# Optimization experiments

Hardware: AMD Instinct MI355X
Metric: run time of the kernel (lower is better)

## Reference

```python
import jax, jax.numpy as jnp
import numpy as np

RADIUS = 0.5
K = 32  # num_neighbor


def ball_query(distances, radius, k):
    # distances: (B, M, N) squared distances; mark points outside radius with N,
    # then sort indices so in-range points (in original order) come first.
    B, M, N = distances.shape
    idx = jnp.where(distances >= radius ** 2, N,
                    jnp.arange(N, dtype=jnp.int32)[None, None, :])
    return jnp.sort(idx, axis=-1)[:, :, :k]  # (B, M, k), padded with N


def setup_inputs() -> dict:
    key = jax.random.key(0)
    ks = jax.random.split(key, 6)
    B, N, M, D, C = 4, 16384, 1024, 3, 64
    C_op, C_out = 64, 128
    positions = jax.random.normal(ks[0], (B, N, D), jnp.float32)
    features = jax.random.normal(ks[1], (B, N, C), jnp.float32)
    centers = jax.random.normal(ks[2], (B, M, D), jnp.float32)
    distances = jax.random.uniform(ks[3], (B, M, N), dtype=jnp.float32)
    W_op = jax.random.normal(ks[4], (D + C, C_op), jnp.float32) * 0.05
    b_op = jnp.zeros((C_op,), jnp.float32)
    W_agg = jax.random.normal(ks[5], (C_op, C_out), jnp.float32) * 0.05
    b_agg = jnp.zeros((C_out,), jnp.float32)
    return {"positions": positions, "features": features, "centers": centers,
            "distances": distances, "W_op": W_op, "b_op": b_op,
            "W_agg": W_agg, "b_agg": b_agg}


def reference(positions, features, centers, distances, W_op, b_op, W_agg, b_agg):
    B, N, D = positions.shape
    ids = ball_query(distances, RADIUS, K)      # (B, M, K); N marks invalid slot
    mask = ids != N                             # valid neighbor mask
    safe = jnp.where(mask, ids, 0)
    bidx = jnp.arange(B)[:, None, None]
    pos_n = positions[bidx, safe]               # (B, M, K, D) neighbor gather
    feat_n = features[bidx, safe]               # (B, M, K, C)
    rel = pos_n - centers[:, :, None, :]        # relative coordinates
    # NeighborOperator: pointwise linear on [rel_pos, features]
    f = jnp.concatenate([rel, feat_n], axis=-1) @ W_op + b_op  # (B, M, K, C_op)
    # invalid slots map to the zeros row in the torch index_put trick
    f = jnp.where(mask[..., None], f, 0.0)
    pooled = jnp.max(f, axis=2)                 # neighbor max-pool (B, M, C_op)
    # Conv1dBlock with kernel 1 == per-center linear + relu
    return jax.nn.relu(pooled @ W_agg + b_agg)  # (B, M, out_channels)
```

## Files before the change

kernel.cpp:

```cpp
#include <hip/hip_runtime.h>

constexpr int B_   = 4;
constexpr int N_   = 16384;
constexpr int M_   = 1024;
constexpr int C_   = 64;
constexpr int CIN_ = 3 + C_;
constexpr int COP_ = 64;
constexpr int COUT_ = 128;
constexpr int K_   = 32;
constexpr float R2_ = 0.25f;

__global__ __launch_bounds__(64) void pointnet_fused(
    const float* __restrict__ positions,
    const float* __restrict__ features,
    const float* __restrict__ centers,
    const float* __restrict__ distances,
    const float* __restrict__ W_op,
    const float* __restrict__ b_op,
    const float* __restrict__ W_agg,
    const float* __restrict__ b_agg,
    float* __restrict__ out)
{
    const int j  = threadIdx.x;
    const int bm = blockIdx.x;
    const int b  = bm >> 10;

    __shared__ int   s_ids[K_];
    __shared__ float s_pooled[COP_];

    float w[CIN_];
    #pragma unroll
    for (int c = 0; c < CIN_; ++c) w[c] = W_op[c * COP_ + j];
    const float bop_j = b_op[j];

    const float ctr0 = centers[bm * 3 + 0];
    const float ctr1 = centers[bm * 3 + 1];
    const float ctr2 = centers[bm * 3 + 2];

    const float* drow = distances + (size_t)bm * N_;
    int found = 0;
    for (int n0 = 0; n0 < N_ && found < K_; n0 += 64) {
        const float d = drow[n0 + j];
        const bool pred = d < R2_;
        const unsigned long long mask = __ballot(pred);
        const int rank = found + __popcll(mask & ((1ull << j) - 1ull));
        if (pred && rank < K_) s_ids[rank] = n0 + j;
        found += (int)__popcll(mask);
    }
    const int valid = found < K_ ? found : K_;
    __syncthreads();

    float pooled = -INFINITY;
    for (int k = 0; k < valid; ++k) {
        const int id = __builtin_amdgcn_readfirstlane(s_ids[k]);
        const float* pp = positions + ((size_t)b * N_ + id) * 3;
        const float* fp = features  + ((size_t)b * N_ + id) * C_;
        float acc = bop_j;
        acc = fmaf(pp[0] - ctr0, w[0], acc);
        acc = fmaf(pp[1] - ctr1, w[1], acc);
        acc = fmaf(pp[2] - ctr2, w[2], acc);
        #pragma unroll
        for (int c = 0; c < C_; ++c) acc = fmaf(fp[c], w[3 + c], acc);
        pooled = fmaxf(pooled, acc);
    }
    if (valid < K_) pooled = fmaxf(pooled, 0.0f);

    s_pooled[j] = pooled;
    __syncthreads();

    float acc0 = b_agg[j];
    float acc1 = b_agg[j + 64];
    #pragma unroll
    for (int jj = 0; jj < COP_; ++jj) {
        const float p = s_pooled[jj];
        acc0 = fmaf(p, W_agg[jj * COUT_ + j],      acc0);
        acc1 = fmaf(p, W_agg[jj * COUT_ + j + 64], acc1);
    }
    float* orow = out + (size_t)bm * COUT_;
    orow[j]      = fmaxf(acc0, 0.0f);
    orow[j + 64] = fmaxf(acc1, 0.0f);
}

extern "C" void kernel_launch(void* const* d_in, const int* in_sizes, int n_in,
                              void* d_out, int out_size, void* d_ws, size_t ws_size,
                              hipStream_t stream) {
    const float* positions = (const float*)d_in[0];
    const float* features  = (const float*)d_in[1];
    const float* centers   = (const float*)d_in[2];
    const float* distances = (const float*)d_in[3];
    const float* W_op      = (const float*)d_in[4];
    const float* b_op      = (const float*)d_in[5];
    const float* W_agg     = (const float*)d_in[6];
    const float* b_agg     = (const float*)d_in[7];
    float* out = (float*)d_out;

    dim3 grid(B_ * M_);
    dim3 block(64);
    pointnet_fused<<<grid, block, 0, stream>>>(
        positions, features, centers, distances,
        W_op, b_op, W_agg, b_agg, out);
}
```

Before: 341.0 us.

## Stage neighbor features in LDS via coalesced gather and pack four centers per block

Gathers the 32 neighbor feature rows with coalesced per-lane loads into shared memory, plus relative positions, instead of serial scalar loads per channel. The neighbor MLP then reads float4 rows from LDS, and every slot is computed and masked to zero when invalid. Four centers share a 256-thread block, which cuts block count and amortises the weight loads. In exchange it uses more LDS and registers and always computes all 32 slots.

```diff
diff --git a/kernel.cpp b/kernel.cpp
--- a/kernel.cpp
+++ b/kernel.cpp
@@ -1,16 +1,17 @@
 #include <hip/hip_runtime.h>
 
-constexpr int B_   = 4;
-constexpr int N_   = 16384;
-constexpr int M_   = 1024;
-constexpr int C_   = 64;
-constexpr int CIN_ = 3 + C_;
-constexpr int COP_ = 64;
+constexpr int B_    = 4;
+constexpr int N_    = 16384;
+constexpr int M_    = 1024;
+constexpr int C_    = 64;
+constexpr int CIN_  = 68;
+constexpr int COP_  = 64;
 constexpr int COUT_ = 128;
-constexpr int K_   = 32;
+constexpr int K_    = 32;
 constexpr float R2_ = 0.25f;
+constexpr int CPB_  = 4;
 
-__global__ __launch_bounds__(64) void pointnet_fused(
+__global__ __launch_bounds__(256, 4) void pointnet_fused(
     const float* __restrict__ positions,
     const float* __restrict__ features,
     const float* __restrict__ centers,
@@ -21,64 +22,87 @@
     const float* __restrict__ b_agg,
     float* __restrict__ out)
 {
-    const int j  = threadIdx.x;
-    const int bm = blockIdx.x;
-    const int b  = bm >> 10;
+    const int lane = threadIdx.x & 63;
+    const int wv   = threadIdx.x >> 6;
+    const int bm   = blockIdx.x * CPB_ + wv;
+    const int b    = bm >> 10;
 
-    __shared__ int   s_ids[K_];
-    __shared__ float s_pooled[COP_];
+    __shared__ __align__(16) float s_X[CPB_][K_][CIN_];
+    __shared__ int   s_ids[CPB_][K_];
+    __shared__ float s_pooled[CPB_][COP_];
 
-    float w[CIN_];
-    #pragma unroll
-    for (int c = 0; c < CIN_; ++c) w[c] = W_op[c * COP_ + j];
-    const float bop_j = b_op[j];
+    const float* drow = distances + (size_t)bm * N_;
+    if (lane < K_) s_ids[wv][lane] = 0;
+    int found = 0;
+    for (int n0 = 0; n0 < N_ && found < K_; n0 += 64) {
+        const float d = drow[n0 + lane];
+        const bool pred = d < R2_;
+        const unsigned long long m = __ballot(pred);
+        const int rank = found + __popcll(m & ((1ull << lane) - 1ull));
+        if (pred && rank < K_) s_ids[wv][rank] = n0 + lane;
+        found += (int)__popcll(m);
+    }
+    const int valid = found < K_ ? found : K_;
+    __syncthreads();
 
     const float ctr0 = centers[bm * 3 + 0];
     const float ctr1 = centers[bm * 3 + 1];
     const float ctr2 = centers[bm * 3 + 2];
 
-    const float* drow = distances + (size_t)bm * N_;
-    int found = 0;
-    for (int n0 = 0; n0 < N_ && found < K_; n0 += 64) {
-        const float d = drow[n0 + j];
-        const bool pred = d < R2_;
-        const unsigned long long mask = __ballot(pred);
-        const int rank = found + __popcll(mask & ((1ull << j) - 1ull));
-        if (pred && rank < K_) s_ids[rank] = n0 + j;
-        found += (int)__popcll(mask);
+    const int myid = s_ids[wv][lane & (K_ - 1)];
+
+    if (lane < K_) {
+        const float* pp = positions + ((size_t)b * N_ + myid) * 3;
+        s_X[wv][lane][0]  = pp[0] - ctr0;
+        s_X[wv][lane][1]  = pp[1] - ctr1;
+        s_X[wv][lane][2]  = pp[2] - ctr2;
+        s_X[wv][lane][67] = 0.0f;
     }
-    const int valid = found < K_ ? found : K_;
+    #pragma unroll 8
+    for (int k = 0; k < K_; ++k) {
+        const int idk = __shfl(myid, k);
+        const float f = features[((size_t)b * N_ + idk) * C_ + lane];
+        s_X[wv][k][3 + lane] = f;
+    }
     __syncthreads();
 
+    float w[CIN_];
+    #pragma unroll
+    for (int c = 0; c < 67; ++c) w[c] = W_op[c * COP_ + lane];
+    w[67] = 0.0f;
+    const float bop = b_op[lane];
+
+    const float* Xc = &s_X[wv][0][0];
     float pooled = -INFINITY;
-    for (int k = 0; k < valid; ++k) {
-        const int id = __builtin_amdgcn_readfirstlane(s_ids[k]);
-        const float* pp = positions + ((size_t)b * N_ + id) * 3;
-        const float* fp = features  + ((size_t)b * N_ + id) * C_;
-        float acc = bop_j;
-        acc = fmaf(pp[0] - ctr0, w[0], acc);
-        acc = fmaf(pp[1] - ctr1, w[1], acc);
-        acc = fmaf(pp[2] - ctr2, w[2], acc);
+    #pragma unroll 4
+    for (int k = 0; k < K_; ++k) {
+        const float* row = Xc + k * CIN_;
+        float acc = bop;
         #pragma unroll
-        for (int c = 0; c < C_; ++c) acc = fmaf(fp[c], w[3 + c], acc);
+        for (int c = 0; c < CIN_; c += 4) {
+            const float4 x = *(const float4*)(row + c);
+            acc = fmaf(x.x, w[c + 0], acc);
+            acc = fmaf(x.y, w[c + 1], acc);
+            acc = fmaf(x.z, w[c + 2], acc);
+            acc = fmaf(x.w, w[c + 3], acc);
+        }
+        acc = (k < valid) ? acc : 0.0f;
         pooled = fmaxf(pooled, acc);
     }
-    if (valid < K_) pooled = fmaxf(pooled, 0.0f);
-
-    s_pooled[j] = pooled;
+    s_pooled[wv][lane] = pooled;
     __syncthreads();
 
-    float acc0 = b_agg[j];
-    float acc1 = b_agg[j + 64];
+    float a0 = b_agg[lane];
+    float a1 = b_agg[lane + 64];
     #pragma unroll
     for (int jj = 0; jj < COP_; ++jj) {
-        const float p = s_pooled[jj];
-        acc0 = fmaf(p, W_agg[jj * COUT_ + j],      acc0);
-        acc1 = fmaf(p, W_agg[jj * COUT_ + j + 64], acc1);
+        const float p = s_pooled[wv][jj];
+        a0 = fmaf(p, W_agg[jj * COUT_ + lane],      a0);
+        a1 = fmaf(p, W_agg[jj * COUT_ + lane + 64], a1);
     }
     float* orow = out + (size_t)bm * COUT_;
-    orow[j]      = fmaxf(acc0, 0.0f);
-    orow[j + 64] = fmaxf(acc1, 0.0f);
+    orow[lane]      = fmaxf(a0, 0.0f);
+    orow[lane + 64] = fmaxf(a1, 0.0f);
 }
 
 extern "C" void kernel_launch(void* const* d_in, const int* in_sizes, int n_in,
@@ -94,8 +118,8 @@
     const float* b_agg     = (const float*)d_in[7];
     float* out = (float*)d_out;
 
-    dim3 grid(B_ * M_);
-    dim3 block(64);
+    dim3 grid((B_ * M_) / CPB_);
+    dim3 block(64 * CPB_);
     pointnet_fused<<<grid, block, 0, stream>>>(
         positions, features, centers, distances,
         W_op, b_op, W_agg, b_agg, out);
```

After: 513.7 us. +50.6%, slower.
